# Optimization experiments

Measured on AMD Instinct MI355X. Metric: run time of the kernel, lower is better.

The kernel has to match this reference:

```python
import jax, jax.numpy as jnp
import numpy as np

N, D, O = 8000, 9, 1  # mulElements hard-codes 8000 rows; fc: 9 -> 1


def setup_inputs() -> dict:
    key = jax.random.key(0)
    ks = jax.random.split(key, 5)
    # scale x small so the (buggy) cumulative product over 8000 rows stays finite/nonzero
    x = jax.random.normal(ks[0], (N, D), dtype=jnp.float32) * 1e-3
    a1 = jnp.array([1.0], dtype=jnp.float32)
    c1 = jnp.array([0.0], dtype=jnp.float32)
    a2 = jnp.array([1.1], dtype=jnp.float32)
    c2 = jnp.array([5e-4], dtype=jnp.float32)
    w_fc1 = jax.random.normal(ks[1], (O, D), dtype=jnp.float32) / np.sqrt(D)
    b_fc1 = jax.random.normal(ks[2], (O,), dtype=jnp.float32) * 0.01
    w_fc2 = jax.random.normal(ks[3], (O, D), dtype=jnp.float32) / np.sqrt(D)
    b_fc2 = jax.random.normal(ks[4], (O,), dtype=jnp.float32) * 0.01
    return {"x": x, "a1": a1, "c1": c1, "a2": a2, "c2": c2,
            "w_fc1": w_fc1, "b_fc1": b_fc1, "w_fc2": w_fc2, "b_fc2": b_fc2}


def reference(x, a1, c1, a2, c2, w_fc1, b_fc1, w_fc2, b_fc2):
    # Gaussian memberships, [N, D]
    miu1 = jnp.exp(-(((x - c1) / a1) ** 2))
    miu2 = jnp.exp(-(((x - c2) / a2) ** 2))
    # mulElements: w_temp is NOT reset per row in the original code, so
    # w[i] = prod over rows 0..i of the row-product -> cumprod of row products.
    w1 = jnp.cumprod(jnp.prod(miu1, axis=1))  # [N]
    w2 = jnp.cumprod(jnp.prod(miu2, axis=1))  # [N]
    s = w1 + w2
    w1_bar = w1 / s  # [N]
    w2_bar = w2 / s  # [N]
    f1 = x @ w_fc1.T + b_fc1  # [N, 1]
    f2 = x @ w_fc2.T + b_fc2  # [N, 1]
    # torch broadcasting: [N] * [N,1] -> [N,N]
    out = f1 * w1_bar[None, :] + f2 * w2_bar[None, :]  # [N, N]
    return out
```

## Files before the change

kernel.cpp:

```cpp
#include <hip/hip_runtime.h>

#define NROWS 8000
#define DDIM 9
#define NCOL4 (NROWS / 4)

__global__ __launch_bounds__(256)
void anfis_rows(const float* __restrict__ x,
                const float* __restrict__ a1p, const float* __restrict__ c1p,
                const float* __restrict__ a2p, const float* __restrict__ c2p,
                const float* __restrict__ w_fc1, const float* __restrict__ b_fc1,
                const float* __restrict__ w_fc2, const float* __restrict__ b_fc2,
                float* __restrict__ s1o, float* __restrict__ s2o,
                float* __restrict__ f1o, float* __restrict__ f2o) {
    int r = blockIdx.x * 256 + threadIdx.x;
    if (r >= NROWS) return;
    const float inv_a1 = 1.0f / a1p[0];
    const float c1 = c1p[0];
    const float inv_a2 = 1.0f / a2p[0];
    const float c2 = c2p[0];
    float s1 = 0.f, s2 = 0.f, d1 = 0.f, d2 = 0.f;
#pragma unroll
    for (int j = 0; j < DDIM; ++j) {
        float xv = x[r * DDIM + j];
        float t1 = (xv - c1) * inv_a1;
        float t2 = (xv - c2) * inv_a2;
        s1 += t1 * t1;
        s2 += t2 * t2;
        d1 += xv * w_fc1[j];
        d2 += xv * w_fc2[j];
    }
    s1o[r] = s1;
    s2o[r] = s2;
    f1o[r] = d1 + b_fc1[0];
    f2o[r] = d2 + b_fc2[0];
}

#define SCAN_T 1024
#define RPT 8

__global__ __launch_bounds__(SCAN_T)
void anfis_scan(const float* __restrict__ s1, const float* __restrict__ s2,
                float* __restrict__ w1bo, float* __restrict__ w2bo) {
    __shared__ float sh1[SCAN_T];
    __shared__ float sh2[SCAN_T];
    const int t = threadIdx.x;
    const int r0 = t * RPT;

    float cs1[RPT], cs2[RPT];
    float run1 = 0.f, run2 = 0.f;
#pragma unroll
    for (int k = 0; k < RPT; ++k) {
        int r = r0 + k;
        float v1 = 0.f, v2 = 0.f;
        if (r < NROWS) { v1 = s1[r]; v2 = s2[r]; }
        run1 += v1;
        run2 += v2;
        cs1[k] = run1;
        cs2[k] = run2;
    }
    sh1[t] = run1;
    sh2[t] = run2;
    __syncthreads();
    for (int off = 1; off < SCAN_T; off <<= 1) {
        float v1 = 0.f, v2 = 0.f;
        if (t >= off) { v1 = sh1[t - off]; v2 = sh2[t - off]; }
        __syncthreads();
        sh1[t] += v1;
        sh2[t] += v2;
        __syncthreads();
    }
    const float pre1 = (t > 0) ? sh1[t - 1] : 0.f;
    const float pre2 = (t > 0) ? sh2[t - 1] : 0.f;
#pragma unroll
    for (int k = 0; k < RPT; ++k) {
        int r = r0 + k;
        if (r < NROWS) {
            float a = pre1 + cs1[k];
            float b = pre2 + cs2[k];
            float e = expf(a - b);
            float inv = 1.0f / (1.0f + e);
            w1bo[r] = inv;
            w2bo[r] = e * inv;
        }
    }
}

__global__ __launch_bounds__(256)
void anfis_out(const float* __restrict__ f1, const float* __restrict__ f2,
               const float* __restrict__ w1b, const float* __restrict__ w2b,
               float* __restrict__ out) {
    const int j4 = blockIdx.x * 256 + threadIdx.x;
    if (j4 >= NCOL4) return;
    const int i = blockIdx.y;
    const float a = f1[i];
    const float b = f2[i];
    const float4 u = ((const float4*)w1b)[j4];
    const float4 v = ((const float4*)w2b)[j4];
    float4 o;
    o.x = a * u.x + b * v.x;
    o.y = a * u.y + b * v.y;
    o.z = a * u.z + b * v.z;
    o.w = a * u.w + b * v.w;
    ((float4*)out)[(size_t)i * NCOL4 + j4] = o;
}

extern "C" void kernel_launch(void* const* d_in, const int* in_sizes, int n_in,
                              void* d_out, int out_size, void* d_ws, size_t ws_size,
                              hipStream_t stream) {
    const float* x     = (const float*)d_in[0];
    const float* a1    = (const float*)d_in[1];
    const float* c1    = (const float*)d_in[2];
    const float* a2    = (const float*)d_in[3];
    const float* c2    = (const float*)d_in[4];
    const float* w_fc1 = (const float*)d_in[5];
    const float* b_fc1 = (const float*)d_in[6];
    const float* w_fc2 = (const float*)d_in[7];
    const float* b_fc2 = (const float*)d_in[8];
    float* out = (float*)d_out;

    float* ws  = (float*)d_ws;
    float* s1  = ws;
    float* s2  = ws + 8000;
    float* f1  = ws + 16000;
    float* f2  = ws + 24000;
    float* w1b = ws + 32000;
    float* w2b = ws + 40000;

    anfis_rows<<<32, 256, 0, stream>>>(x, a1, c1, a2, c2,
                                       w_fc1, b_fc1, w_fc2, b_fc2,
                                       s1, s2, f1, f2);
    anfis_scan<<<1, SCAN_T, 0, stream>>>(s1, s2, w1b, w2b);
    anfis_out<<<dim3((NCOL4 + 255) / 256, NROWS), 256, 0, stream>>>(f1, f2, w1b, w2b, out);
}
```

Measured before the change: 277.4 us.

## Fuse row prep into scan kernel and batch output rows with nontemporal stores

Merges the per-row membership/linear computation into the single-block scan kernel, which drops one launch and the s1/s2 workspace round trip, and packs f1/f2 into one float2 array. The output kernel now handles 50 rows per block, reusing the loaded w1b/w2b vectors across rows, and writes with nontemporal stores to avoid polluting cache on the 256MB output. The trade-off is that the row computation now runs serially inside one 1024-thread block, and the output grid has far fewer blocks.

```diff
diff --git a/kernel.cpp b/kernel.cpp
--- a/kernel.cpp
+++ b/kernel.cpp
@@ -3,58 +3,56 @@
 #define NROWS 8000
 #define DDIM 9
 #define NCOL4 (NROWS / 4)
+#define ROWS_PER_BLK 50
+#define SCAN_T 1024
+#define RPT 8
 
-__global__ __launch_bounds__(256)
-void anfis_rows(const float* __restrict__ x,
+typedef float f32x4 __attribute__((ext_vector_type(4)));
+
+__global__ __launch_bounds__(SCAN_T)
+void anfis_prep(const float* __restrict__ x,
                 const float* __restrict__ a1p, const float* __restrict__ c1p,
                 const float* __restrict__ a2p, const float* __restrict__ c2p,
                 const float* __restrict__ w_fc1, const float* __restrict__ b_fc1,
                 const float* __restrict__ w_fc2, const float* __restrict__ b_fc2,
-                float* __restrict__ s1o, float* __restrict__ s2o,
-                float* __restrict__ f1o, float* __restrict__ f2o) {
-    int r = blockIdx.x * 256 + threadIdx.x;
-    if (r >= NROWS) return;
+                float* __restrict__ w1bo, float* __restrict__ w2bo,
+                float2* __restrict__ f12o) {
+    __shared__ float sh1[SCAN_T];
+    __shared__ float sh2[SCAN_T];
+    const int t = threadIdx.x;
+    const int r0 = t * RPT;
+
     const float inv_a1 = 1.0f / a1p[0];
     const float c1 = c1p[0];
     const float inv_a2 = 1.0f / a2p[0];
     const float c2 = c2p[0];
-    float s1 = 0.f, s2 = 0.f, d1 = 0.f, d2 = 0.f;
+    const float bb1 = b_fc1[0];
+    const float bb2 = b_fc2[0];
+    float wf1[DDIM], wf2[DDIM];
 #pragma unroll
-    for (int j = 0; j < DDIM; ++j) {
-        float xv = x[r * DDIM + j];
-        float t1 = (xv - c1) * inv_a1;
-        float t2 = (xv - c2) * inv_a2;
-        s1 += t1 * t1;
-        s2 += t2 * t2;
-        d1 += xv * w_fc1[j];
-        d2 += xv * w_fc2[j];
-    }
-    s1o[r] = s1;
-    s2o[r] = s2;
-    f1o[r] = d1 + b_fc1[0];
-    f2o[r] = d2 + b_fc2[0];
-}
-
-#define SCAN_T 1024
-#define RPT 8
-
-__global__ __launch_bounds__(SCAN_T)
-void anfis_scan(const float* __restrict__ s1, const float* __restrict__ s2,
-                float* __restrict__ w1bo, float* __restrict__ w2bo) {
-    __shared__ float sh1[SCAN_T];
-    __shared__ float sh2[SCAN_T];
-    const int t = threadIdx.x;
-    const int r0 = t * RPT;
+    for (int j = 0; j < DDIM; ++j) { wf1[j] = w_fc1[j]; wf2[j] = w_fc2[j]; }
 
     float cs1[RPT], cs2[RPT];
     float run1 = 0.f, run2 = 0.f;
 #pragma unroll
     for (int k = 0; k < RPT; ++k) {
         int r = r0 + k;
-        float v1 = 0.f, v2 = 0.f;
-        if (r < NROWS) { v1 = s1[r]; v2 = s2[r]; }
-        run1 += v1;
-        run2 += v2;
+        float s1 = 0.f, s2 = 0.f, d1 = 0.f, d2 = 0.f;
+        if (r < NROWS) {
+#pragma unroll
+            for (int j = 0; j < DDIM; ++j) {
+                float xv = x[r * DDIM + j];
+                float t1 = (xv - c1) * inv_a1;
+                float t2 = (xv - c2) * inv_a2;
+                s1 += t1 * t1;
+                s2 += t2 * t2;
+                d1 += xv * wf1[j];
+                d2 += xv * wf2[j];
+            }
+            f12o[r] = make_float2(d1 + bb1, d2 + bb2);
+        }
+        run1 += s1;
+        run2 += s2;
         cs1[k] = run1;
         cs2[k] = run2;
     }
@@ -86,22 +84,24 @@
 }
 
 __global__ __launch_bounds__(256)
-void anfis_out(const float* __restrict__ f1, const float* __restrict__ f2,
+void anfis_out(const float2* __restrict__ f12,
                const float* __restrict__ w1b, const float* __restrict__ w2b,
                float* __restrict__ out) {
     const int j4 = blockIdx.x * 256 + threadIdx.x;
     if (j4 >= NCOL4) return;
-    const int i = blockIdx.y;
-    const float a = f1[i];
-    const float b = f2[i];
-    const float4 u = ((const float4*)w1b)[j4];
-    const float4 v = ((const float4*)w2b)[j4];
-    float4 o;
-    o.x = a * u.x + b * v.x;
-    o.y = a * u.y + b * v.y;
-    o.z = a * u.z + b * v.z;
-    o.w = a * u.w + b * v.w;
-    ((float4*)out)[(size_t)i * NCOL4 + j4] = o;
+    const int i0 = blockIdx.y * ROWS_PER_BLK;
+
+    const f32x4 u = ((const f32x4*)w1b)[j4];
+    const f32x4 v = ((const f32x4*)w2b)[j4];
+    f32x4* orow = (f32x4*)out + (size_t)i0 * NCOL4 + j4;
+
+#pragma unroll 2
+    for (int k = 0; k < ROWS_PER_BLK; ++k) {
+        const float2 ab = f12[i0 + k];
+        f32x4 o = ab.x * u + ab.y * v;
+        __builtin_nontemporal_store(o, orow);
+        orow += NCOL4;
+    }
 }
 
 extern "C" void kernel_launch(void* const* d_in, const int* in_sizes, int n_in,
@@ -118,17 +118,14 @@
     const float* b_fc2 = (const float*)d_in[8];
     float* out = (float*)d_out;
 
-    float* ws  = (float*)d_ws;
-    float* s1  = ws;
-    float* s2  = ws + 8000;
-    float* f1  = ws + 16000;
-    float* f2  = ws + 24000;
-    float* w1b = ws + 32000;
-    float* w2b = ws + 40000;
+    float* ws   = (float*)d_ws;
+    float* w1b  = ws;
+    float* w2b  = ws + 8000;
+    float2* f12 = (float2*)(ws + 16000);
 
-    anfis_rows<<<32, 256, 0, stream>>>(x, a1, c1, a2, c2,
-                                       w_fc1, b_fc1, w_fc2, b_fc2,
-                                       s1, s2, f1, f2);
-    anfis_scan<<<1, SCAN_T, 0, stream>>>(s1, s2, w1b, w2b);
-    anfis_out<<<dim3((NCOL4 + 255) / 256, NROWS), 256, 0, stream>>>(f1, f2, w1b, w2b, out);
+    anfis_prep<<<1, SCAN_T, 0, stream>>>(x, a1, c1, a2, c2,
+                                         w_fc1, b_fc1, w_fc2, b_fc2,
+                                         w1b, w2b, f12);
+    anfis_out<<<dim3((NCOL4 + 255) / 256, NROWS / ROWS_PER_BLK), 256, 0, stream>>>(
+        f12, w1b, w2b, out);
 }
```

After: 306.4 us. 10.5% more time.
